# Performance work log

Measured on AMD Instinct MI355X. Metric: run time of the kernel, lower is better.

## Reference

```python
import jax, jax.numpy as jnp
import numpy as np

IN_FEATURES = 1024
FEATURES = 1024
GRID_SIZE = 5
SPLINE_ORDER = 3
GRID_MIN, GRID_MAX = -2.0, 2.0
EPS = 1e-7


def setup_inputs() -> dict:
    key = jax.random.key(0)
    k_x, k_w, k_ss, k_bs = jax.random.split(key, 4)
    x = jax.random.normal(k_x, (4096, IN_FEATURES), dtype=jnp.float32)
    # Extended knot sequence: grid_size + 2*spline_order + 1 knots
    h = (GRID_MAX - GRID_MIN) / GRID_SIZE
    grid = GRID_MIN + h * jnp.arange(-SPLINE_ORDER, GRID_SIZE + SPLINE_ORDER + 1,
                                     dtype=jnp.float32)  # (12,)
    K = GRID_SIZE + SPLINE_ORDER  # number of B-spline basis functions = 8
    # glorot_uniform over (I, O, K)
    limit = float(np.sqrt(6.0 / (IN_FEATURES + FEATURES)))
    spline_weight = jax.random.uniform(k_w, (IN_FEATURES, FEATURES, K),
                                       minval=-limit, maxval=limit, dtype=jnp.float32)
    spline_scaler = jax.random.uniform(k_ss, (IN_FEATURES, FEATURES),
                                       minval=-limit, maxval=limit, dtype=jnp.float32)
    base_scaler = jax.random.uniform(k_bs, (IN_FEATURES, FEATURES),
                                     minval=-limit, maxval=limit, dtype=jnp.float32)
    return {"x": x, "grid": grid, "spline_weight": spline_weight,
            "spline_scaler": spline_scaler, "base_scaler": base_scaler}


def _bspline_bases(x, grid):
    # x: (B, I); grid: (G+2S+1,) -> bases: (B, I, G+S)
    xe = x[..., None]
    # order-0 indicator bases on each knot interval
    bases = ((xe >= grid[:-1]) & (xe < grid[1:])).astype(x.dtype)
    for p in range(1, SPLINE_ORDER + 1):  # Cox-de Boor recursion
        left = (xe - grid[:-(p + 1)]) / (grid[p:-1] - grid[:-(p + 1)] + EPS)
        right = (grid[p + 1:] - xe) / (grid[p + 1:] - grid[1:-p] + EPS)
        bases = left * bases[..., :-1] + right * bases[..., 1:]
    return bases


def reference(x, grid, spline_weight, spline_scaler, base_scaler):
    # Base path: b(x) = swish(x) = x * sigmoid(x), summed over inputs with base_scaler
    base_out = jnp.einsum('bi,io->bo', x * jax.nn.sigmoid(x), base_scaler)
    # Spline path: per-connection spline with per-connection scaling
    bases = _bspline_bases(x, grid)                       # (B, I, K)
    scaled_w = spline_weight * spline_scaler[..., None]   # (I, O, K)
    spline_out = jnp.einsum('bik,iok->bo', bases, scaled_w)
    return base_out + spline_out
```

## Files before the change

kernel.cpp:

```cpp
#include <hip/hip_runtime.h>
#include <hip/hip_bf16.h>
#include <cstdint>
#include <cstddef>

#define I_F   1024
#define O_F   1024
#define BATCH 4096
#define KDIM  9216
#define EPSC  1e-7f

typedef __bf16 bf16;
typedef __bf16 bf16x4 __attribute__((ext_vector_type(4)));
typedef __bf16 bf16x8 __attribute__((ext_vector_type(8)));
typedef float  f32x4  __attribute__((ext_vector_type(4)));

__global__ __launch_bounds__(256) void act_kernel(const float* __restrict__ x,
                                                  const float* __restrict__ grid,
                                                  bf16* __restrict__ A) {
    int t  = blockIdx.x * 256 + threadIdx.x;
    int b  = t >> 8;
    int i0 = (t & 255) << 2;
    f32x4 xv4 = *(const f32x4*)(x + (size_t)b * I_F + i0);

    float g[12];
#pragma unroll
    for (int j = 0; j < 12; ++j) g[j] = grid[j];
    float r1[11], r2[10], r3[9];
#pragma unroll
    for (int j = 0; j < 11; ++j) r1[j] = __builtin_amdgcn_rcpf(g[j + 1] - g[j] + EPSC);
#pragma unroll
    for (int j = 0; j < 10; ++j) r2[j] = __builtin_amdgcn_rcpf(g[j + 2] - g[j] + EPSC);
#pragma unroll
    for (int j = 0; j < 9;  ++j) r3[j] = __builtin_amdgcn_rcpf(g[j + 3] - g[j] + EPSC);

    float sw[4];
    float bs8[4][8];
#pragma unroll
    for (int e = 0; e < 4; ++e) {
        float xv = xv4[e];
        float bas[11];
#pragma unroll
        for (int j = 0; j < 11; ++j)
            bas[j] = (xv >= g[j] && xv < g[j + 1]) ? 1.0f : 0.0f;
#pragma unroll
        for (int j = 0; j < 10; ++j)
            bas[j] = (xv - g[j]) * r1[j] * bas[j] + (g[j + 2] - xv) * r1[j + 1] * bas[j + 1];
#pragma unroll
        for (int j = 0; j < 9; ++j)
            bas[j] = (xv - g[j]) * r2[j] * bas[j] + (g[j + 3] - xv) * r2[j + 1] * bas[j + 1];
#pragma unroll
        for (int j = 0; j < 8; ++j)
            bas[j] = (xv - g[j]) * r3[j] * bas[j] + (g[j + 4] - xv) * r3[j + 1] * bas[j + 1];
#pragma unroll
        for (int k = 0; k < 8; ++k) bs8[e][k] = bas[k];
        float sig = 1.0f / (1.0f + __expf(-xv));
        sw[e] = xv * sig;
    }

    bf16* outp = A + (size_t)b * KDIM + i0;
    *(bf16x4*)(outp) = (bf16x4){(bf16)sw[0], (bf16)sw[1], (bf16)sw[2], (bf16)sw[3]};
#pragma unroll
    for (int k = 0; k < 8; ++k)
        *(bf16x4*)(outp + (size_t)(k + 1) * 1024) =
            (bf16x4){(bf16)bs8[0][k], (bf16)bs8[1][k], (bf16)bs8[2][k], (bf16)bs8[3][k]};
}

__global__ __launch_bounds__(256) void wprep_kernel(const float* __restrict__ w,
                                                    const float* __restrict__ ss,
                                                    const float* __restrict__ bs,
                                                    bf16* __restrict__ Wt) {
    int g = blockIdx.x * 256 + threadIdx.x;
    int i  = g & 1023;
    int o0 = (g >> 10) << 3;
    size_t io0 = (size_t)i * 1024 + o0;
    f32x4 ssv0 = *(const f32x4*)(ss + io0);
    f32x4 ssv1 = *(const f32x4*)(ss + io0 + 4);
    f32x4 bsv0 = *(const f32x4*)(bs + io0);
    f32x4 bsv1 = *(const f32x4*)(bs + io0 + 4);
#pragma unroll
    for (int oo = 0; oo < 8; ++oo) {
        int o = o0 + oo;
        float scale = (oo < 4) ? ssv0[oo & 3] : ssv1[oo & 3];
        float base  = (oo < 4) ? bsv0[oo & 3] : bsv1[oo & 3];
        const float* wp = w + (io0 + oo) * 8;
        f32x4 w0 = *(const f32x4*)(wp);
        f32x4 w1 = *(const f32x4*)(wp + 4);

        bf16* outp = Wt + (size_t)o * KDIM + i;
        outp[0] = (bf16)base;
#pragma unroll
        for (int k = 0; k < 4; ++k) outp[(size_t)(k + 1) * 1024] = (bf16)(w0[k] * scale);
#pragma unroll
        for (int k = 0; k < 4; ++k) outp[(size_t)(k + 5) * 1024] = (bf16)(w1[k] * scale);
    }
}

__device__ __forceinline__ void load_lds16(const bf16* g, bf16* l) {
    __builtin_amdgcn_global_load_lds(
        (__attribute__((address_space(1))) void*)g,
        (__attribute__((address_space(3))) void*)l, 16, 0, 0);
}

__global__ __launch_bounds__(512, 2) void gemm_kernel(const bf16* __restrict__ A,
                                                      const bf16* __restrict__ Wt,
                                                      bf16* __restrict__ parts,
                                                      int split, int ktiles) {
    __shared__ __align__(16) bf16 SA[4][8192];
    __shared__ __align__(16) bf16 SB[4][8192];

    const int t    = threadIdx.x;
    const int lane = t & 63;
    const int w    = t >> 6;

    const int nwg8 = gridDim.x >> 3;
    const int L    = (blockIdx.x & 7) * nwg8 + (blockIdx.x >> 3);
    const int nper = split << 4;
    const int tn   = L / nper;
    const int rem  = L - tn * nper;
    const int s    = rem >> 4;
    const int tm   = rem & 15;

    const int row0 = tm << 8;
    const int col0 = tn << 8;
    const size_t k0 = (size_t)s * ktiles * 32;

    const int sr = lane >> 2;
    const int lc = (lane & 3) ^ ((lane >> 3) & 3);
    const bf16* gA0 = A  + (size_t)(row0 + w * 16 + sr) * KDIM + k0 + lc * 8;
    const bf16* gB0 = Wt + (size_t)(col0 + w * 16 + sr) * KDIM + k0 + lc * 8;

    const int wm  = w >> 2;
    const int wn  = w & 3;
    const int r15 = lane & 15;
    const int g4  = lane >> 4;
    const int swb = (r15 >> 1) & 3;
    const int cp  = ((g4 ^ swb) << 3);

    f32x4 acc[8][4];
#pragma unroll
    for (int mt = 0; mt < 8; ++mt)
#pragma unroll
        for (int nt = 0; nt < 4; ++nt) acc[mt][nt] = (f32x4){0.f, 0.f, 0.f, 0.f};

    auto stage = [&](int j) {
        const int sl = j & 3;
        const bf16* pa = gA0 + (size_t)j * 32;
        const bf16* pb = gB0 + (size_t)j * 32;
        load_lds16(pa,                      &SA[sl][w * 512]);
        load_lds16(pa + (size_t)128 * KDIM, &SA[sl][4096 + w * 512]);
        load_lds16(pb,                      &SB[sl][w * 512]);
        load_lds16(pb + (size_t)128 * KDIM, &SB[sl][4096 + w * 512]);
    };

    auto frag_load = [&](int sl, bf16x8 (&af)[8], bf16x8 (&bv)[4]) {
        af[0] = *(const bf16x8*)&SA[sl][(wm * 128 + 0 * 16 + r15) * 32 + cp];
#pragma unroll
        for (int nt = 0; nt < 4; ++nt)
            bv[nt] = *(const bf16x8*)&SB[sl][(wn * 64 + nt * 16 + r15) * 32 + cp];
#pragma unroll
        for (int mt = 1; mt < 8; ++mt)
            af[mt] = *(const bf16x8*)&SA[sl][(wm * 128 + mt * 16 + r15) * 32 + cp];
    };

    auto do_mfma = [&](bf16x8 (&af)[8], bf16x8 (&bv)[4]) {
        __builtin_amdgcn_s_setprio(1);
#pragma unroll
        for (int mt = 0; mt < 8; ++mt)
#pragma unroll
            for (int nt = 0; nt < 4; ++nt)
                acc[mt][nt] = __builtin_amdgcn_mfma_f32_16x16x32_bf16(
                    af[mt], bv[nt], acc[mt][nt], 0, 0, 0);
        __builtin_amdgcn_s_setprio(0);
    };

    stage(0); stage(1); stage(2);

    int j = 0;
    for (; j < ktiles - 3; ++j) {
        asm volatile("s_waitcnt vmcnt(8)" ::: "memory");
        __builtin_amdgcn_s_barrier();
        asm volatile("" ::: "memory");
        bf16x8 af[8], bv[4];
        frag_load(j & 3, af, bv);
        stage(j + 3);
        do_mfma(af, bv);
    }
    {
        asm volatile("s_waitcnt vmcnt(8)" ::: "memory");
        __builtin_amdgcn_s_barrier();
        asm volatile("" ::: "memory");
        bf16x8 af[8], bv[4];
        frag_load(j & 3, af, bv);
        do_mfma(af, bv);
        ++j;
    }
    {
        asm volatile("s_waitcnt vmcnt(4)" ::: "memory");
        __builtin_amdgcn_s_barrier();
        asm volatile("" ::: "memory");
        bf16x8 af[8], bv[4];
        frag_load(j & 3, af, bv);
        do_mfma(af, bv);
        ++j;
    }
    {
        asm volatile("s_waitcnt vmcnt(0)" ::: "memory");
        __builtin_amdgcn_s_barrier();
        asm volatile("" ::: "memory");
        bf16x8 af[8], bv[4];
        frag_load(j & 3, af, bv);
        do_mfma(af, bv);
    }

    bf16* cp2 = parts + (size_t)s * BATCH * O_F
              + (size_t)(row0 + wm * 128) * O_F + col0 + wn * 64 + r15;
#pragma unroll
    for (int mt = 0; mt < 8; ++mt)
#pragma unroll
        for (int nt = 0; nt < 4; ++nt)
#pragma unroll
            for (int r = 0; r < 4; ++r)
                cp2[(size_t)(mt * 16 + g4 * 4 + r) * O_F + nt * 16] = (bf16)acc[mt][nt][r];
}

__global__ __launch_bounds__(256) void add_kernel(float* __restrict__ out,
                                                  const bf16* __restrict__ parts,
                                                  int np) {
    int t = blockIdx.x * 256 + threadIdx.x;
    f32x4 a = {0.f, 0.f, 0.f, 0.f};
    for (int p = 0; p < np; ++p) {
        bf16x4 b = *((const bf16x4*)(parts + (size_t)p * BATCH * O_F) + t);
#pragma unroll
        for (int e = 0; e < 4; ++e) a[e] += (float)b[e];
    }
    *((f32x4*)out + t) = a;
}

extern "C" void kernel_launch(void* const* d_in, const int* in_sizes, int n_in,
                              void* d_out, int out_size, void* d_ws, size_t ws_size,
                              hipStream_t stream) {
    const float* x    = (const float*)d_in[0];
    const float* grid = (const float*)d_in[1];
    const float* w    = (const float*)d_in[2];
    const float* ss   = (const float*)d_in[3];
    const float* bs   = (const float*)d_in[4];
    float* out = (float*)d_out;

    const size_t nA = (size_t)BATCH * KDIM * 2;
    const size_t nW = (size_t)O_F   * KDIM * 2;
    const size_t nP = (size_t)BATCH * O_F  * 2;

    bf16* A  = (bf16*)d_ws;
    bf16* Wt = (bf16*)((char*)d_ws + nA);
    bf16* parts = (bf16*)((char*)d_ws + nA + nW);

    act_kernel<<<(BATCH * I_F / 4) / 256, 256, 0, stream>>>(x, grid, A);
    wprep_kernel<<<(I_F * O_F / 8) / 256, 256, 0, stream>>>(w, ss, bs, Wt);

    int split = (ws_size >= nA + nW + 4 * nP) ? 4
              : (ws_size >= nA + nW + 2 * nP) ? 2 : 1;
    gemm_kernel<<<64 * split, 512, 0, stream>>>(A, Wt, parts, split, 288 / split);
    add_kernel<<<(BATCH * O_F / 4) / 256, 256, 0, stream>>>(out, parts, split);
}
```

Baseline: 118.7 us.

## Merge prep kernels and switch GEMM to BK=64 double-buffered LDS pipeline

The activation and weight-prep kernels are fused into one launch, with block ranges split between the two jobs. The GEMM moves from a 4-stage, BK=32 LDS ring to a 2-stage, BK=64 double buffer with a wider XOR swizzle. Each iteration now does two MFMA sub-steps per barrier and waits on vmcnt(0). This halves barrier count and the number of k-iterations, but the prefetch depth is shallower, so global load latency is more exposed. Launch bounds drop to 1 block per CU, which may reduce latency hiding.

```diff
diff --git a/kernel.cpp b/kernel.cpp
--- a/kernel.cpp
+++ b/kernel.cpp
@@ -14,84 +14,85 @@
 typedef __bf16 bf16x8 __attribute__((ext_vector_type(8)));
 typedef float  f32x4  __attribute__((ext_vector_type(4)));
 
-__global__ __launch_bounds__(256) void act_kernel(const float* __restrict__ x,
-                                                  const float* __restrict__ grid,
-                                                  bf16* __restrict__ A) {
-    int t  = blockIdx.x * 256 + threadIdx.x;
-    int b  = t >> 8;
-    int i0 = (t & 255) << 2;
-    f32x4 xv4 = *(const f32x4*)(x + (size_t)b * I_F + i0);
-
-    float g[12];
-#pragma unroll
-    for (int j = 0; j < 12; ++j) g[j] = grid[j];
-    float r1[11], r2[10], r3[9];
-#pragma unroll
-    for (int j = 0; j < 11; ++j) r1[j] = __builtin_amdgcn_rcpf(g[j + 1] - g[j] + EPSC);
-#pragma unroll
-    for (int j = 0; j < 10; ++j) r2[j] = __builtin_amdgcn_rcpf(g[j + 2] - g[j] + EPSC);
-#pragma unroll
-    for (int j = 0; j < 9;  ++j) r3[j] = __builtin_amdgcn_rcpf(g[j + 3] - g[j] + EPSC);
-
-    float sw[4];
-    float bs8[4][8];
-#pragma unroll
-    for (int e = 0; e < 4; ++e) {
-        float xv = xv4[e];
-        float bas[11];
-#pragma unroll
-        for (int j = 0; j < 11; ++j)
-            bas[j] = (xv >= g[j] && xv < g[j + 1]) ? 1.0f : 0.0f;
-#pragma unroll
-        for (int j = 0; j < 10; ++j)
-            bas[j] = (xv - g[j]) * r1[j] * bas[j] + (g[j + 2] - xv) * r1[j + 1] * bas[j + 1];
-#pragma unroll
-        for (int j = 0; j < 9; ++j)
-            bas[j] = (xv - g[j]) * r2[j] * bas[j] + (g[j + 3] - xv) * r2[j + 1] * bas[j + 1];
-#pragma unroll
-        for (int j = 0; j < 8; ++j)
-            bas[j] = (xv - g[j]) * r3[j] * bas[j] + (g[j + 4] - xv) * r3[j + 1] * bas[j + 1];
-#pragma unroll
-        for (int k = 0; k < 8; ++k) bs8[e][k] = bas[k];
-        float sig = 1.0f / (1.0f + __expf(-xv));
-        sw[e] = xv * sig;
-    }
-
-    bf16* outp = A + (size_t)b * KDIM + i0;
-    *(bf16x4*)(outp) = (bf16x4){(bf16)sw[0], (bf16)sw[1], (bf16)sw[2], (bf16)sw[3]};
-#pragma unroll
-    for (int k = 0; k < 8; ++k)
-        *(bf16x4*)(outp + (size_t)(k + 1) * 1024) =
-            (bf16x4){(bf16)bs8[0][k], (bf16)bs8[1][k], (bf16)bs8[2][k], (bf16)bs8[3][k]};
-}
-
-__global__ __launch_bounds__(256) void wprep_kernel(const float* __restrict__ w,
-                                                    const float* __restrict__ ss,
-                                                    const float* __restrict__ bs,
-                                                    bf16* __restrict__ Wt) {
-    int g = blockIdx.x * 256 + threadIdx.x;
-    int i  = g & 1023;
-    int o0 = (g >> 10) << 3;
-    size_t io0 = (size_t)i * 1024 + o0;
-    f32x4 ssv0 = *(const f32x4*)(ss + io0);
-    f32x4 ssv1 = *(const f32x4*)(ss + io0 + 4);
-    f32x4 bsv0 = *(const f32x4*)(bs + io0);
-    f32x4 bsv1 = *(const f32x4*)(bs + io0 + 4);
-#pragma unroll
-    for (int oo = 0; oo < 8; ++oo) {
-        int o = o0 + oo;
-        float scale = (oo < 4) ? ssv0[oo & 3] : ssv1[oo & 3];
-        float base  = (oo < 4) ? bsv0[oo & 3] : bsv1[oo & 3];
-        const float* wp = w + (io0 + oo) * 8;
-        f32x4 w0 = *(const f32x4*)(wp);
-        f32x4 w1 = *(const f32x4*)(wp + 4);
-
-        bf16* outp = Wt + (size_t)o * KDIM + i;
-        outp[0] = (bf16)base;
-#pragma unroll
-        for (int k = 0; k < 4; ++k) outp[(size_t)(k + 1) * 1024] = (bf16)(w0[k] * scale);
-#pragma unroll
-        for (int k = 0; k < 4; ++k) outp[(size_t)(k + 5) * 1024] = (bf16)(w1[k] * scale);
+__global__ __launch_bounds__(256) void prep_kernel(const float* __restrict__ x,
+                                                   const float* __restrict__ grid,
+                                                   const float* __restrict__ w,
+                                                   const float* __restrict__ ss,
+                                                   const float* __restrict__ bs,
+                                                   bf16* __restrict__ A,
+                                                   bf16* __restrict__ Wt) {
+    if (blockIdx.x < 512) {
+        int g = blockIdx.x * 256 + threadIdx.x;
+        int i  = g & 1023;
+        int o0 = (g >> 10) << 3;
+        size_t io0 = (size_t)i * 1024 + o0;
+        f32x4 ssv0 = *(const f32x4*)(ss + io0);
+        f32x4 ssv1 = *(const f32x4*)(ss + io0 + 4);
+        f32x4 bsv0 = *(const f32x4*)(bs + io0);
+        f32x4 bsv1 = *(const f32x4*)(bs + io0 + 4);
+#pragma unroll
+        for (int oo = 0; oo < 8; ++oo) {
+            int o = o0 + oo;
+            float scale = (oo < 4) ? ssv0[oo & 3] : ssv1[oo & 3];
+            float base  = (oo < 4) ? bsv0[oo & 3] : bsv1[oo & 3];
+            const float* wp = w + (io0 + oo) * 8;
+            f32x4 w0 = *(const f32x4*)(wp);
+            f32x4 w1 = *(const f32x4*)(wp + 4);
+
+            bf16* outp = Wt + (size_t)o * KDIM + i;
+            outp[0] = (bf16)base;
+#pragma unroll
+            for (int k = 0; k < 4; ++k) outp[(size_t)(k + 1) * 1024] = (bf16)(w0[k] * scale);
+#pragma unroll
+            for (int k = 0; k < 4; ++k) outp[(size_t)(k + 5) * 1024] = (bf16)(w1[k] * scale);
+        }
+    } else {
+        int t  = (blockIdx.x - 512) * 256 + threadIdx.x;
+        int b  = t >> 8;
+        int i0 = (t & 255) << 2;
+        f32x4 xv4 = *(const f32x4*)(x + (size_t)b * I_F + i0);
+
+        float g[12];
+#pragma unroll
+        for (int j = 0; j < 12; ++j) g[j] = grid[j];
+        float r1[11], r2[10], r3[9];
+#pragma unroll
+        for (int j = 0; j < 11; ++j) r1[j] = __builtin_amdgcn_rcpf(g[j + 1] - g[j] + EPSC);
+#pragma unroll
+        for (int j = 0; j < 10; ++j) r2[j] = __builtin_amdgcn_rcpf(g[j + 2] - g[j] + EPSC);
+#pragma unroll
+        for (int j = 0; j < 9;  ++j) r3[j] = __builtin_amdgcn_rcpf(g[j + 3] - g[j] + EPSC);
+
+        float sw[4];
+        float bs8[4][8];
+#pragma unroll
+        for (int e = 0; e < 4; ++e) {
+            float xv = xv4[e];
+            float bas[11];
+#pragma unroll
+            for (int j = 0; j < 11; ++j)
+                bas[j] = (xv >= g[j] && xv < g[j + 1]) ? 1.0f : 0.0f;
+#pragma unroll
+            for (int j = 0; j < 10; ++j)
+                bas[j] = (xv - g[j]) * r1[j] * bas[j] + (g[j + 2] - xv) * r1[j + 1] * bas[j + 1];
+#pragma unroll
+            for (int j = 0; j < 9; ++j)
+                bas[j] = (xv - g[j]) * r2[j] * bas[j] + (g[j + 3] - xv) * r2[j + 1] * bas[j + 1];
+#pragma unroll
+            for (int j = 0; j < 8; ++j)
+                bas[j] = (xv - g[j]) * r3[j] * bas[j] + (g[j + 4] - xv) * r3[j + 1] * bas[j + 1];
+#pragma unroll
+            for (int k = 0; k < 8; ++k) bs8[e][k] = bas[k];
+            float sig = 1.0f / (1.0f + __expf(-xv));
+            sw[e] = xv * sig;
+        }
+
+        bf16* outp = A + (size_t)b * KDIM + i0;
+        *(bf16x4*)(outp) = (bf16x4){(bf16)sw[0], (bf16)sw[1], (bf16)sw[2], (bf16)sw[3]};
+#pragma unroll
+        for (int k = 0; k < 8; ++k)
+            *(bf16x4*)(outp + (size_t)(k + 1) * 1024) =
+                (bf16x4){(bf16)bs8[0][k], (bf16)bs8[1][k], (bf16)bs8[2][k], (bf16)bs8[3][k]};
     }
 }
 
@@ -101,12 +102,12 @@
         (__attribute__((address_space(3))) void*)l, 16, 0, 0);
 }
 
-__global__ __launch_bounds__(512, 2) void gemm_kernel(const bf16* __restrict__ A,
+__global__ __launch_bounds__(512, 1) void gemm_kernel(const bf16* __restrict__ A,
                                                       const bf16* __restrict__ Wt,
                                                       bf16* __restrict__ parts,
                                                       int split, int ktiles) {
-    __shared__ __align__(16) bf16 SA[4][8192];
-    __shared__ __align__(16) bf16 SB[4][8192];
+    __shared__ __align__(16) bf16 SA[2][16384];
+    __shared__ __align__(16) bf16 SB[2][16384];
 
     const int t    = threadIdx.x;
     const int lane = t & 63;
@@ -122,19 +123,18 @@
 
     const int row0 = tm << 8;
     const int col0 = tn << 8;
-    const size_t k0 = (size_t)s * ktiles * 32;
-
-    const int sr = lane >> 2;
-    const int lc = (lane & 3) ^ ((lane >> 3) & 3);
-    const bf16* gA0 = A  + (size_t)(row0 + w * 16 + sr) * KDIM + k0 + lc * 8;
-    const bf16* gB0 = Wt + (size_t)(col0 + w * 16 + sr) * KDIM + k0 + lc * 8;
+    const size_t k0 = (size_t)s * ktiles * 64;
+
+    const int sr8 = lane >> 3;
+    const int lc  = (lane & 7) ^ sr8;
+    const bf16* gA0 = A  + (size_t)(row0 + w * 32 + sr8) * KDIM + k0 + lc * 8;
+    const bf16* gB0 = Wt + (size_t)(col0 + w * 32 + sr8) * KDIM + k0 + lc * 8;
 
     const int wm  = w >> 2;
     const int wn  = w & 3;
     const int r15 = lane & 15;
     const int g4  = lane >> 4;
-    const int swb = (r15 >> 1) & 3;
-    const int cp  = ((g4 ^ swb) << 3);
+    const int rx7 = r15 & 7;
 
     f32x4 acc[8][4];
 #pragma unroll
@@ -143,23 +143,26 @@
         for (int nt = 0; nt < 4; ++nt) acc[mt][nt] = (f32x4){0.f, 0.f, 0.f, 0.f};
 
     auto stage = [&](int j) {
-        const int sl = j & 3;
-        const bf16* pa = gA0 + (size_t)j * 32;
-        const bf16* pb = gB0 + (size_t)j * 32;
-        load_lds16(pa,                      &SA[sl][w * 512]);
-        load_lds16(pa + (size_t)128 * KDIM, &SA[sl][4096 + w * 512]);
-        load_lds16(pb,                      &SB[sl][w * 512]);
-        load_lds16(pb + (size_t)128 * KDIM, &SB[sl][4096 + w * 512]);
+        const int sl = j & 1;
+        const bf16* pa = gA0 + (size_t)j * 64;
+        const bf16* pb = gB0 + (size_t)j * 64;
+#pragma unroll
+        for (int q = 0; q < 4; ++q)
+            load_lds16(pa + (size_t)(q * 8) * KDIM, &SA[sl][(w * 32 + q * 8) * 64]);
+#pragma unroll
+        for (int q = 0; q < 4; ++q)
+            load_lds16(pb + (size_t)(q * 8) * KDIM, &SB[sl][(w * 32 + q * 8) * 64]);
     };
 
-    auto frag_load = [&](int sl, bf16x8 (&af)[8], bf16x8 (&bv)[4]) {
-        af[0] = *(const bf16x8*)&SA[sl][(wm * 128 + 0 * 16 + r15) * 32 + cp];
+    auto frag_load = [&](int sl, int ks, bf16x8 (&af)[8], bf16x8 (&bv)[4]) {
+        const int cp = (((ks * 4 + g4) ^ rx7) << 3);
+        af[0] = *(const bf16x8*)&SA[sl][(wm * 128 + 0 * 16 + r15) * 64 + cp];
 #pragma unroll
         for (int nt = 0; nt < 4; ++nt)
-            bv[nt] = *(const bf16x8*)&SB[sl][(wn * 64 + nt * 16 + r15) * 32 + cp];
+            bv[nt] = *(const bf16x8*)&SB[sl][(wn * 64 + nt * 16 + r15) * 64 + cp];
 #pragma unroll
         for (int mt = 1; mt < 8; ++mt)
-            af[mt] = *(const bf16x8*)&SA[sl][(wm * 128 + mt * 16 + r15) * 32 + cp];
+            af[mt] = *(const bf16x8*)&SA[sl][(wm * 128 + mt * 16 + r15) * 64 + cp];
     };
 
     auto do_mfma = [&](bf16x8 (&af)[8], bf16x8 (&bv)[4]) {
@@ -173,43 +176,18 @@
         __builtin_amdgcn_s_setprio(0);
     };
 
-    stage(0); stage(1); stage(2);
-
-    int j = 0;
-    for (; j < ktiles - 3; ++j) {
-        asm volatile("s_waitcnt vmcnt(8)" ::: "memory");
-        __builtin_amdgcn_s_barrier();
-        asm volatile("" ::: "memory");
-        bf16x8 af[8], bv[4];
-        frag_load(j & 3, af, bv);
-        stage(j + 3);
-        do_mfma(af, bv);
-    }
-    {
-        asm volatile("s_waitcnt vmcnt(8)" ::: "memory");
-        __builtin_amdgcn_s_barrier();
-        asm volatile("" ::: "memory");
-        bf16x8 af[8], bv[4];
-        frag_load(j & 3, af, bv);
-        do_mfma(af, bv);
-        ++j;
-    }
-    {
-        asm volatile("s_waitcnt vmcnt(4)" ::: "memory");
-        __builtin_amdgcn_s_barrier();
-        asm volatile("" ::: "memory");
-        bf16x8 af[8], bv[4];
-        frag_load(j & 3, af, bv);
-        do_mfma(af, bv);
-        ++j;
-    }
-    {
+    stage(0);
+
+    for (int j = 0; j < ktiles; ++j) {
         asm volatile("s_waitcnt vmcnt(0)" ::: "memory");
         __builtin_amdgcn_s_barrier();
         asm volatile("" ::: "memory");
-        bf16x8 af[8], bv[4];
-        frag_load(j & 3, af, bv);
-        do_mfma(af, bv);
+        bf16x8 af0[8], bv0[4], af1[8], bv1[4];
+        frag_load(j & 1, 0, af0, bv0);
+        if (j + 1 < ktiles) stage(j + 1);
+        do_mfma(af0, bv0);
+        frag_load(j & 1, 1, af1, bv1);
+        do_mfma(af1, bv1);
     }
 
     bf16* cp2 = parts + (size_t)s * BATCH * O_F
@@ -254,11 +232,10 @@
     bf16* Wt = (bf16*)((char*)d_ws + nA);
     bf16* parts = (bf16*)((char*)d_ws + nA + nW);
 
-    act_kernel<<<(BATCH * I_F / 4) / 256, 256, 0, stream>>>(x, grid, A);
-    wprep_kernel<<<(I_F * O_F / 8) / 256, 256, 0, stream>>>(w, ss, bs, Wt);
+    prep_kernel<<<4608, 256, 0, stream>>>(x, grid, w, ss, bs, A, Wt);
 
     int split = (ws_size >= nA + nW + 4 * nP) ? 4
               : (ws_size >= nA + nW + 2 * nP) ? 2 : 1;
-    gemm_kernel<<<64 * split, 512, 0, stream>>>(A, Wt, parts, split, 288 / split);
+    gemm_kernel<<<64 * split, 512, 0, stream>>>(A, Wt, parts, split, 144 / split);
     add_kernel<<<(BATCH * O_F / 4) / 256, 256, 0, stream>>>(out, parts, split);
 }
```

After: 109.6 us. -7.7%, faster.
